# Kernel tuning notes

Hardware: AMD Instinct MI355X
Metric: run time of the kernel (lower is better)

## Reference

```python
import jax, jax.numpy as jnp
import numpy as np

B, S, E = 2, 2048, 1024
N_HEADS = 16
HEAD_DIM = E // N_HEADS  # 64
ATTN_SCALE = 1.0 / np.sqrt(E)  # NOTE: original scales by 1/sqrt(hidden_dim_phi), not head_dim
ROPE_BASE = 10000.0


def _rope(t):
    # t: (B, H, S, D) with D = HEAD_DIM; interleaved-pair RoPE (torchtune-style)
    d = t.shape[-1]
    s = t.shape[-2]
    inv_freq = 1.0 / (ROPE_BASE ** (jnp.arange(0, d, 2, dtype=jnp.float32) / d))  # (D/2,)
    ang = jnp.arange(s, dtype=jnp.float32)[:, None] * inv_freq[None, :]  # (S, D/2)
    cos, sin = jnp.cos(ang), jnp.sin(ang)  # (S, D/2)
    tp = t.reshape(t.shape[:-1] + (d // 2, 2))
    te, to = tp[..., 0], tp[..., 1]  # (B,H,S,D/2)
    oe = te * cos - to * sin
    oo = te * sin + to * cos
    return jnp.stack([oe, oo], axis=-1).reshape(t.shape)


def setup_inputs() -> dict:
    key = jax.random.key(0)
    ks = jax.random.split(key, 5)
    std = 0.02
    return {
        "x": jax.random.normal(ks[0], (B, S, E), dtype=jnp.float32),
        "W_q": jax.random.normal(ks[1], (E, E), dtype=jnp.float32) * std,
        "W_k": jax.random.normal(ks[2], (E, E), dtype=jnp.float32) * std,
        "W_v": jax.random.normal(ks[3], (E, E), dtype=jnp.float32) * std,
        "W_o": jax.random.normal(ks[4], (E, E), dtype=jnp.float32) * std,
    }


def reference(x, W_q, W_k, W_v, W_o):
    b, s, e = x.shape
    hd = e // N_HEADS
    # projections -> (B, H, S, D)
    def proj(w):
        return (x @ w).reshape(b, s, N_HEADS, hd).transpose(0, 2, 1, 3)
    q = _rope(proj(W_q))
    k = _rope(proj(W_k))
    v = proj(W_v)
    scores = jnp.einsum('bhsd,bhtd->bhst', q, k) * ATTN_SCALE  # (B,H,S,S)
    causal = jnp.triu(jnp.ones((s, s), dtype=bool), k=1)
    scores = jnp.where(causal, -jnp.inf, scores)
    probs = jax.nn.softmax(scores, axis=-1)  # dropout is identity in eval mode
    out = jnp.einsum('bhst,bhtd->bhsd', probs, v)
    out = out.transpose(0, 2, 1, 3).reshape(b, s, e)
    return out @ W_o
```

## Files before the change

kernel.cpp:

```cpp
#include <hip/hip_runtime.h>
#include <hip/hip_bf16.h>

#define S_LEN 2048
#define E_DIM 1024
#define NH 16
#define HD 64
#define ATTN_SCALE 0.03125f
#define QSCALE_L2E 0.045084312f
#define KVB 128

typedef __attribute__((ext_vector_type(8))) short short8;
typedef __attribute__((ext_vector_type(8))) unsigned short ushort8;
typedef __attribute__((ext_vector_type(4))) unsigned short ushort4_t;
typedef __attribute__((ext_vector_type(4))) float f32x4;
typedef __attribute__((ext_vector_type(4))) float f4;
typedef __attribute__((ext_vector_type(2))) unsigned int uint2_t;

__device__ __forceinline__ float bf2f(unsigned short u) {
    unsigned int x = ((unsigned int)u) << 16;
    return __builtin_bit_cast(float, x);
}
__device__ __forceinline__ unsigned short f2bf(float f) {
    unsigned int x = __builtin_bit_cast(unsigned int, f);
    x += 0x7FFFu + ((x >> 16) & 1u);
    return (unsigned short)(x >> 16);
}
__device__ __forceinline__ float exp2_fast(float x) {
    float r;
    asm("v_exp_f32 %0, %1" : "=v"(r) : "v"(x));
    return r;
}
__device__ __forceinline__ void gload16(const unsigned short* g, unsigned short* l) {
    __builtin_amdgcn_global_load_lds(
        (__attribute__((address_space(1))) void*)g,
        (__attribute__((address_space(3))) void*)l, 16, 0, 0);
}

__global__ __launch_bounds__(256) void k_convert(const float* __restrict__ x,
                                                 unsigned short* __restrict__ xb) {
    size_t i = ((size_t)blockIdx.x * 256 + threadIdx.x) * 8;
    f4 a = *(const f4*)(x + i);
    f4 b = *(const f4*)(x + i + 4);
    ushort8 o;
    o[0] = f2bf(a[0]); o[1] = f2bf(a[1]); o[2] = f2bf(a[2]); o[3] = f2bf(a[3]);
    o[4] = f2bf(b[0]); o[5] = f2bf(b[1]); o[6] = f2bf(b[2]); o[7] = f2bf(b[3]);
    *(ushort8*)(xb + i) = o;
}

__global__ __launch_bounds__(256) void k_transw(const float* W0, const float* W1,
                                                const float* W2, const float* W3,
                                                unsigned short* T0, unsigned short* T1,
                                                unsigned short* T2, unsigned short* T3) {
    const float* W; unsigned short* T;
    switch (blockIdx.z) {
        case 0: W = W0; T = T0; break;
        case 1: W = W1; T = T1; break;
        case 2: W = W2; T = T2; break;
        default: W = W3; T = T3; break;
    }
    __shared__ float tile[32][33];
    int tx = threadIdx.x, ty = threadIdx.y;
    int bx = blockIdx.x * 32, by = blockIdx.y * 32;
#pragma unroll
    for (int i = 0; i < 4; i++)
        tile[ty + i * 8][tx] = W[(size_t)(by + ty + i * 8) * E_DIM + bx + tx];
    __syncthreads();
#pragma unroll
    for (int i = 0; i < 4; i++)
        T[(size_t)(bx + ty + i * 8) * E_DIM + by + tx] = f2bf(tile[tx][ty + i * 8]);
}

__global__ __launch_bounds__(256) void k_rope_table(float* __restrict__ cosT,
                                                    float* __restrict__ sinT) {
    int idx = blockIdx.x * 256 + threadIdx.x;
    int s = idx >> 5, j = idx & 31;
    float inv = expf(-(float)j * (9.210340371976184f / 32.f));
    float ang = (float)s * inv;
    cosT[idx] = cosf(ang);
    sinT[idx] = sinf(ang);
}

template <int BM, int BN, int NBN, bool QKV3>
__global__ __launch_bounds__(256, 3)
void k_gemmN(const unsigned short* __restrict__ A,
             const unsigned short* __restrict__ B,
             unsigned short* __restrict__ Qo,
             unsigned short* __restrict__ Ko,
             unsigned short* __restrict__ Vto,
             float* __restrict__ Fo,
             const float* __restrict__ cosT,
             const float* __restrict__ sinT) {
    constexpr int THREADS = 256;
    constexpr int WM = BM / 2, WN = BN / 2;
    constexpr int FM = WM / 16, FN = WN / 16;
    constexpr int NT = E_DIM / 64;
    constexpr int AR = BM * 8 / THREADS;
    constexpr int BR = BN * 8 / THREADS;
    constexpr int STG = AR + BR;
    constexpr int NWG = (4096 / BM) * NBN;
    __shared__ unsigned short Al[2][BM * 64];
    __shared__ unsigned short Bl[2][BN * 64];
    int tid = threadIdx.x, lane = tid & 63, wid = tid >> 6;
    int l15 = lane & 15, lg = lane >> 4;
    int wr = wid >> 1, wc = wid & 1;
    int orig = blockIdx.y * NBN + blockIdx.x;
    int wg = (orig & 7) * (NWG / 8) + (orig >> 3);
    int bm = wg / NBN, bn = wg % NBN;

    auto stage = [&](int buf, int k0) {
#pragma unroll
        for (int i = 0; i < AR; i++) {
            int r = i * (THREADS / 8) + wid * 8 + (lane >> 3);
            int cs = (lane & 7) ^ (r & 7);
            gload16(A + (size_t)(bm * BM + r) * E_DIM + k0 + cs * 8,
                    &Al[buf][i * (THREADS * 8) + wid * 512]);
        }
#pragma unroll
        for (int i = 0; i < BR; i++) {
            int r = i * (THREADS / 8) + wid * 8 + (lane >> 3);
            int cs = (lane & 7) ^ (r & 7);
            gload16(B + (size_t)(bn * BN + r) * E_DIM + k0 + cs * 8,
                    &Bl[buf][i * (THREADS * 8) + wid * 512]);
        }
    };

    f32x4 acc[FM][FN] = {};
    stage(0, 0);
    for (int t = 0; t < NT; t++) {
        int cur = t & 1;
        if (t + 1 < NT) {
            stage(cur ^ 1, (t + 1) * 64);
            asm volatile("s_waitcnt vmcnt(%0)" :: "n"(STG) : "memory");
        } else {
            asm volatile("s_waitcnt vmcnt(0)" ::: "memory");
        }
        __builtin_amdgcn_s_barrier();
        __builtin_amdgcn_sched_barrier(0);
#pragma unroll
        for (int ks = 0; ks < 2; ks++) {
            short8 af[FM], bfv[FN];
#pragma unroll
            for (int m = 0; m < FM; m++) {
                int r = wr * WM + m * 16 + l15;
                int gc = ks * 4 + lg;
                af[m] = *(const short8*)&Al[cur][r * 64 + ((gc ^ (r & 7)) << 3)];
            }
#pragma unroll
            for (int n = 0; n < FN; n++) {
                int r = wc * WN + n * 16 + l15;
                int gc = ks * 4 + lg;
                bfv[n] = *(const short8*)&Bl[cur][r * 64 + ((gc ^ (r & 7)) << 3)];
            }
            __builtin_amdgcn_s_setprio(1);
#pragma unroll
            for (int m = 0; m < FM; m++)
#pragma unroll
                for (int n = 0; n < FN; n++)
                    acc[m][n] = __builtin_amdgcn_mfma_f32_16x16x32_bf16(
                        af[m], bfv[n], acc[m][n], 0, 0, 0);
            __builtin_amdgcn_s_setprio(0);
        }
        __builtin_amdgcn_s_barrier();
    }
#pragma unroll
    for (int m = 0; m < FM; m++) {
        int r0 = bm * BM + wr * WM + m * 16 + lg * 4;
#pragma unroll
        for (int n = 0; n < FN; n++) {
            int colg = bn * BN + wc * WN + n * 16 + l15;
            if (QKV3) {
                int z = colg >> 10, c1 = colg & 1023;
                if (z == 2) {
                    int h = c1 >> 6, d = c1 & 63;
                    int bb = r0 >> 11, s = r0 & 2047;
                    ushort4_t p;
#pragma unroll
                    for (int r = 0; r < 4; r++) p[r] = f2bf(acc[m][n][r]);
                    *(ushort4_t*)(Vto + (((size_t)((bb * 16 + h) * 64 + d)) << 11) + s) = p;
                } else {
                    unsigned short* T = z ? Ko : Qo;
                    int dl = c1 & 63, j = dl >> 1;
                    float sgn = (dl & 1) ? 1.f : -1.f;
                    float scq = z ? 1.f : QSCALE_L2E;
#pragma unroll
                    for (int r = 0; r < 4; r++) {
                        int row = r0 + r, s = row & 2047;
                        float c = cosT[s * 32 + j], sn = sinT[s * 32 + j];
                        float v = acc[m][n][r];
                        float p = __shfl_xor(v, 1);
                        T[(size_t)row * E_DIM + c1] = f2bf((v * c + sgn * p * sn) * scq);
                    }
                }
            } else {
#pragma unroll
                for (int r = 0; r < 4; r++)
                    Fo[(size_t)(r0 + r) * E_DIM + colg] = acc[m][n][r];
            }
        }
    }
}

__global__ __launch_bounds__(256, 2) void k_attn(const unsigned short* __restrict__ Q,
                                                 const unsigned short* __restrict__ K,
                                                 const unsigned short* __restrict__ Vt,
                                                 unsigned short* __restrict__ O) {
    __shared__ unsigned short K_lds[128 * 64];
    __shared__ unsigned short V_lds[64 * 128];
    __shared__ unsigned short P_lds[4][16][136];
    int tid = threadIdx.x, lane = tid & 63, wid = tid >> 6;
    int l15 = lane & 15, lg = lane >> 4;
    int orig = blockIdx.y * 16 + blockIdx.x;
    int wg = (orig & 7) * 64 + (orig >> 3);
    int jp = wg & 15, bh = wg >> 4;
    int b = bh >> 4, h = bh & 15;
    const size_t base_qk = (size_t)b * S_LEN * E_DIM + (size_t)h * HD;
    const unsigned short* Vbh = Vt + ((size_t)(bh * 64) << 11);

    auto stageK = [&](int kt) {
        const unsigned short* Kb = K + base_qk + (size_t)(kt * KVB) * E_DIM;
#pragma unroll
        for (int i = 0; i < 4; i++) {
            int r = i * 32 + wid * 8 + (lane >> 3);
            int cs = (lane & 7) ^ (r & 7);
            gload16(Kb + (size_t)r * E_DIM + cs * 8, K_lds + i * 2048 + wid * 512);
        }
    };
    auto stageV = [&](int kt) {
#pragma unroll
        for (int i = 0; i < 4; i++) {
            int r = i * 16 + wid * 4 + (lane >> 4);
            int cs = (lane & 15) ^ (r & 7);
            gload16(Vbh + (size_t)r * 2048 + kt * KVB + cs * 8,
                    V_lds + i * 2048 + wid * 512);
        }
    };

    for (int pass = 0; pass < 2; ++pass) {
        int qt = pass ? (31 - jp) : jp;
        const unsigned short* Qb = Q + base_qk + (size_t)(qt * 64 + wid * 16) * E_DIM;
        short8 bq[2];
#pragma unroll
        for (int s2 = 0; s2 < 2; s2++)
            bq[s2] = *(const short8*)(Qb + (size_t)l15 * E_DIM + s2 * 32 + lg * 8);
        f32x4 acc_o[4] = {};
        float m_i = -1e30f, l_i = 0.f;
        int q_glob = qt * 64 + wid * 16 + l15;
        int nkt = (qt + 2) >> 1;
        stageK(0);
        stageV(0);
        asm volatile("s_waitcnt vmcnt(4)" ::: "memory");
        __builtin_amdgcn_s_barrier();
        __builtin_amdgcn_sched_barrier(0);
        for (int kt = 0; kt < nkt; ++kt) {
            f32x4 acc_s[8] = {};
            __builtin_amdgcn_s_setprio(1);
#pragma unroll
            for (int mf = 0; mf < 8; mf++) {
                int rK = mf * 16 + l15;
#pragma unroll
                for (int s2 = 0; s2 < 2; s2++) {
                    int gc = s2 * 4 + lg;
                    short8 a = *(const short8*)&K_lds[rK * 64 + ((gc ^ (rK & 7)) << 3)];
                    acc_s[mf] = __builtin_amdgcn_mfma_f32_16x16x32_bf16(
                        a, bq[s2], acc_s[mf], 0, 0, 0);
                }
            }
            __builtin_amdgcn_s_setprio(0);
            __builtin_amdgcn_s_barrier();
            if (kt + 1 < nkt) stageK(kt + 1);
            float sv[32];
            float vmax = -1e30f;
            if (kt == nkt - 1) {
#pragma unroll
                for (int mf = 0; mf < 8; mf++)
#pragma unroll
                    for (int r = 0; r < 4; r++) {
                        int kg = kt * KVB + mf * 16 + lg * 4 + r;
                        float v = acc_s[mf][r];
                        if (kg > q_glob) v = -1e30f;
                        sv[mf * 4 + r] = v;
                        vmax = fmaxf(vmax, v);
                    }
            } else {
#pragma unroll
                for (int mf = 0; mf < 8; mf++)
#pragma unroll
                    for (int r = 0; r < 4; r++) {
                        float v = acc_s[mf][r];
                        sv[mf * 4 + r] = v;
                        vmax = fmaxf(vmax, v);
                    }
            }
            vmax = fmaxf(vmax, __shfl_xor(vmax, 16));
            vmax = fmaxf(vmax, __shfl_xor(vmax, 32));
            float m_new = fmaxf(m_i, vmax);
            float corr = exp2_fast(m_i - m_new);
            float rowsum = 0.f;
#pragma unroll
            for (int i = 0; i < 32; i++) {
                float p = exp2_fast(sv[i] - m_new);
                sv[i] = p;
                rowsum += p;
            }
            rowsum += __shfl_xor(rowsum, 16);
            rowsum += __shfl_xor(rowsum, 32);
            l_i = l_i * corr + rowsum;
            m_i = m_new;
#pragma unroll
            for (int mf = 0; mf < 8; mf++) {
                unsigned int w0, w1;
                asm("v_cvt_pk_bf16_f32 %0, %1, %2"
                    : "=v"(w0) : "v"(sv[mf * 4 + 0]), "v"(sv[mf * 4 + 1]));
                asm("v_cvt_pk_bf16_f32 %0, %1, %2"
                    : "=v"(w1) : "v"(sv[mf * 4 + 2]), "v"(sv[mf * 4 + 3]));
                uint2_t w; w[0] = w0; w[1] = w1;
                *(uint2_t*)&P_lds[wid][l15][mf * 16 + lg * 4] = w;
            }
#pragma unroll
            for (int r = 0; r < 4; r++) {
                float c4 = __shfl(corr, lg * 4 + r);
#pragma unroll
                for (int nf = 0; nf < 4; nf++) acc_o[nf][r] *= c4;
            }
            if (kt + 1 < nkt)
                asm volatile("s_waitcnt vmcnt(4)" ::: "memory");
            else
                asm volatile("s_waitcnt vmcnt(0)" ::: "memory");
            __builtin_amdgcn_s_barrier();
            __builtin_amdgcn_sched_barrier(0);
            __builtin_amdgcn_s_setprio(1);
#pragma unroll
            for (int s2 = 0; s2 < 4; s2++) {
                short8 pa = *(const short8*)&P_lds[wid][l15][s2 * 32 + lg * 8];
#pragma unroll
                for (int nf = 0; nf < 4; nf++) {
                    int rV = nf * 16 + l15;
                    int gc = s2 * 4 + lg;
                    short8 bv = *(const short8*)&V_lds[rV * 128 + ((gc ^ (rV & 7)) << 3)];
                    acc_o[nf] = __builtin_amdgcn_mfma_f32_16x16x32_bf16(
                        pa, bv, acc_o[nf], 0, 0, 0);
                }
            }
            __builtin_amdgcn_s_setprio(0);
            __builtin_amdgcn_s_barrier();
            if (kt + 1 < nkt) {
                stageV(kt + 1);
                asm volatile("s_waitcnt vmcnt(4)" ::: "memory");
            }
            __builtin_amdgcn_s_barrier();
            __builtin_amdgcn_sched_barrier(0);
        }
        unsigned short* Ob = O + base_qk + (size_t)(qt * 64 + wid * 16) * E_DIM;
#pragma unroll
        for (int r = 0; r < 4; r++) {
            float linv = 1.f / __shfl(l_i, lg * 4 + r);
#pragma unroll
            for (int nf = 0; nf < 4; nf++)
                Ob[(size_t)(lg * 4 + r) * E_DIM + nf * 16 + l15] =
                    f2bf(acc_o[nf][r] * linv);
        }
    }
}

extern "C" void kernel_launch(void* const* d_in, const int* in_sizes, int n_in,
                              void* d_out, int out_size, void* d_ws, size_t ws_size,
                              hipStream_t stream) {
    (void)in_sizes; (void)n_in; (void)out_size; (void)ws_size;
    const float* x  = (const float*)d_in[0];
    const float* Wq = (const float*)d_in[1];
    const float* Wk = (const float*)d_in[2];
    const float* Wv = (const float*)d_in[3];
    const float* Wo = (const float*)d_in[4];

    unsigned short* us = (unsigned short*)d_ws;
    unsigned short* xb    = us;
    unsigned short* WqkvT = us + 4194304;
    unsigned short* WoT   = us + 7340032;
    unsigned short* Qb    = us + 8388608;
    unsigned short* Kb    = us + 12582912;
    unsigned short* Vt    = us + 16777216;
    unsigned short* AO    = us + 20971520;
    float* cosT = (float*)((char*)d_ws + 50331648);
    float* sinT = cosT + 65536;

    k_convert<<<2048, 256, 0, stream>>>(x, xb);
    k_transw<<<dim3(32, 32, 4), dim3(32, 8), 0, stream>>>(
        Wq, Wk, Wv, Wo, WqkvT, WqkvT + 1048576, WqkvT + 2097152, WoT);
    k_rope_table<<<256, 256, 0, stream>>>(cosT, sinT);
    k_gemmN<128, 64, 48, true><<<dim3(48, 32), 256, 0, stream>>>(
        xb, WqkvT, Qb, Kb, Vt, nullptr, cosT, sinT);
    k_attn<<<dim3(16, 32), 256, 0, stream>>>(Qb, Kb, Vt, AO);
    k_gemmN<128, 64, 16, false><<<dim3(16, 32), 256, 0, stream>>>(
        AO, WoT, nullptr, nullptr, nullptr, (float*)d_out, cosT, sinT);
}
```

Baseline: 107.4 us.

## Replace QKV projection GEMM with 128x128 tile kernel using direct-to-LDS loads

The fused QKV projection moves to a dedicated kernel with 128x128 output tiles, a K-step of 32, and gload16 copies from global memory straight into single-buffered LDS. Bigger tiles raise arithmetic intensity and halve the workgroup count. In exchange it drops the double-buffered pipelining and adds two barriers per K-step, so load latency may be less hidden. The output-projection GEMM is split into its own simplified template with no other change in behaviour.

```diff
diff --git a/kernel.cpp b/kernel.cpp
--- a/kernel.cpp
+++ b/kernel.cpp
@@ -80,16 +80,95 @@
     sinT[idx] = sinf(ang);
 }
 
-template <int BM, int BN, int NBN, bool QKV3>
 __global__ __launch_bounds__(256, 3)
-void k_gemmN(const unsigned short* __restrict__ A,
+void k_gemm97(const unsigned short* __restrict__ A,
+              const unsigned short* __restrict__ B,
+              unsigned short* __restrict__ Qo,
+              unsigned short* __restrict__ Ko,
+              unsigned short* __restrict__ Vto,
+              const float* __restrict__ cosT,
+              const float* __restrict__ sinT) {
+    constexpr int NBN = 24;
+    constexpr int NWG = 32 * NBN;
+    __shared__ unsigned short Alds[4096];
+    __shared__ unsigned short Blds[4096];
+    int tid = threadIdx.x, lane = tid & 63, wid = tid >> 6;
+    int l15 = lane & 15, lg = lane >> 4;
+    int wr = wid >> 1, wc = wid & 1;
+    int orig = blockIdx.y * NBN + blockIdx.x;
+    int wg = (orig & 7) * (NWG / 8) + (orig >> 3);
+    int bm = wg / NBN, bn = wg % NBN;
+    int c0 = wid * 2, c1c = wid * 2 + 1;
+    int srow0 = c0 * 16 + (lane >> 2);
+    int srow1 = c1c * 16 + (lane >> 2);
+    int scol = (lane & 3) * 8;
+    const unsigned short* As0 = A + (size_t)(bm * 128 + srow0) * E_DIM + scol;
+    const unsigned short* As1 = A + (size_t)(bm * 128 + srow1) * E_DIM + scol;
+    const unsigned short* Bs0 = B + (size_t)(bn * 128 + srow0) * E_DIM + scol;
+    const unsigned short* Bs1 = B + (size_t)(bn * 128 + srow1) * E_DIM + scol;
+    unsigned short* Ad0 = Alds + c0 * 512;
+    unsigned short* Ad1 = Alds + c1c * 512;
+    unsigned short* Bd0 = Blds + c0 * 512;
+    unsigned short* Bd1 = Blds + c1c * 512;
+    f32x4 acc[4][4] = {};
+    for (int k0 = 0; k0 < E_DIM; k0 += 32) {
+        gload16(As0 + k0, Ad0);
+        gload16(As1 + k0, Ad1);
+        gload16(Bs0 + k0, Bd0);
+        gload16(Bs1 + k0, Bd1);
+        __syncthreads();
+        short8 af[4], bfr[4];
+#pragma unroll
+        for (int mf = 0; mf < 4; mf++)
+            af[mf] = *(const short8*)(Alds + (wr * 64 + mf * 16 + l15) * 32 + lg * 8);
+#pragma unroll
+        for (int nf = 0; nf < 4; nf++)
+            bfr[nf] = *(const short8*)(Blds + (wc * 64 + nf * 16 + l15) * 32 + lg * 8);
+#pragma unroll
+        for (int mf = 0; mf < 4; mf++)
+#pragma unroll
+            for (int nf = 0; nf < 4; nf++)
+                acc[mf][nf] = __builtin_amdgcn_mfma_f32_16x16x32_bf16(
+                    af[mf], bfr[nf], acc[mf][nf], 0, 0, 0);
+        __syncthreads();
+    }
+#pragma unroll
+    for (int mf = 0; mf < 4; mf++) {
+        int r0 = bm * 128 + wr * 64 + mf * 16 + lg * 4;
+#pragma unroll
+        for (int nf = 0; nf < 4; nf++) {
+            int colg = bn * 128 + wc * 64 + nf * 16 + l15;
+            int z = colg >> 10, c1 = colg & 1023;
+            if (z == 2) {
+                int h = c1 >> 6, d = c1 & 63;
+                int bb = r0 >> 11, s = r0 & 2047;
+                ushort4_t p;
+#pragma unroll
+                for (int r = 0; r < 4; r++) p[r] = f2bf(acc[mf][nf][r]);
+                *(ushort4_t*)(Vto + (((size_t)((bb * 16 + h) * 64 + d)) << 11) + s) = p;
+            } else {
+                unsigned short* T = z ? Ko : Qo;
+                int dl = c1 & 63, j = dl >> 1;
+                float sgn = (dl & 1) ? 1.f : -1.f;
+                float scq = z ? 1.f : QSCALE_L2E;
+#pragma unroll
+                for (int r = 0; r < 4; r++) {
+                    int row = r0 + r, s = row & 2047;
+                    float c = cosT[s * 32 + j], sn = sinT[s * 32 + j];
+                    float v = acc[mf][nf][r];
+                    float p = __shfl_xor(v, 1);
+                    T[(size_t)row * E_DIM + c1] = f2bf((v * c + sgn * p * sn) * scq);
+                }
+            }
+        }
+    }
+}
+
+template <int BM, int BN, int NBN>
+__global__ __launch_bounds__(256, 3)
+void k_gemmo(const unsigned short* __restrict__ A,
              const unsigned short* __restrict__ B,
-             unsigned short* __restrict__ Qo,
-             unsigned short* __restrict__ Ko,
-             unsigned short* __restrict__ Vto,
-             float* __restrict__ Fo,
-             const float* __restrict__ cosT,
-             const float* __restrict__ sinT) {
+             float* __restrict__ Fo) {
     constexpr int THREADS = 256;
     constexpr int WM = BM / 2, WN = BN / 2;
     constexpr int FM = WM / 16, FN = WN / 16;
@@ -168,34 +247,9 @@
 #pragma unroll
         for (int n = 0; n < FN; n++) {
             int colg = bn * BN + wc * WN + n * 16 + l15;
-            if (QKV3) {
-                int z = colg >> 10, c1 = colg & 1023;
-                if (z == 2) {
-                    int h = c1 >> 6, d = c1 & 63;
-                    int bb = r0 >> 11, s = r0 & 2047;
-                    ushort4_t p;
-#pragma unroll
-                    for (int r = 0; r < 4; r++) p[r] = f2bf(acc[m][n][r]);
-                    *(ushort4_t*)(Vto + (((size_t)((bb * 16 + h) * 64 + d)) << 11) + s) = p;
-                } else {
-                    unsigned short* T = z ? Ko : Qo;
-                    int dl = c1 & 63, j = dl >> 1;
-                    float sgn = (dl & 1) ? 1.f : -1.f;
-                    float scq = z ? 1.f : QSCALE_L2E;
-#pragma unroll
-                    for (int r = 0; r < 4; r++) {
-                        int row = r0 + r, s = row & 2047;
-                        float c = cosT[s * 32 + j], sn = sinT[s * 32 + j];
-                        float v = acc[m][n][r];
-                        float p = __shfl_xor(v, 1);
-                        T[(size_t)row * E_DIM + c1] = f2bf((v * c + sgn * p * sn) * scq);
-                    }
-                }
-            } else {
-#pragma unroll
-                for (int r = 0; r < 4; r++)
-                    Fo[(size_t)(r0 + r) * E_DIM + colg] = acc[m][n][r];
-            }
+#pragma unroll
+            for (int r = 0; r < 4; r++)
+                Fo[(size_t)(r0 + r) * E_DIM + colg] = acc[m][n][r];
         }
     }
 }
@@ -387,9 +441,7 @@
     k_transw<<<dim3(32, 32, 4), dim3(32, 8), 0, stream>>>(
         Wq, Wk, Wv, Wo, WqkvT, WqkvT + 1048576, WqkvT + 2097152, WoT);
     k_rope_table<<<256, 256, 0, stream>>>(cosT, sinT);
-    k_gemmN<128, 64, 48, true><<<dim3(48, 32), 256, 0, stream>>>(
-        xb, WqkvT, Qb, Kb, Vt, nullptr, cosT, sinT);
+    k_gemm97<<<dim3(24, 32), 256, 0, stream>>>(xb, WqkvT, Qb, Kb, Vt, cosT, sinT);
     k_attn<<<dim3(16, 32), 256, 0, stream>>>(Qb, Kb, Vt, AO);
-    k_gemmN<128, 64, 16, false><<<dim3(16, 32), 256, 0, stream>>>(
-        AO, WoT, nullptr, nullptr, nullptr, (float*)d_out, cosT, sinT);
-}
+    k_gemmo<128, 64, 16><<<dim3(16, 32), 256, 0, stream>>>(AO, WoT, (float*)d_out);
+}
```

New measurement: 107.5 us. No clear change (+0.1%).
